# Kernel tuning notes

Hardware: AMD Instinct MI355X
Metric: run time of the kernel (lower is better)

## Reference

```python
import jax, jax.numpy as jnp
import numpy as np

B, S, D, H, E = 2, 1024, 1024, 4096, 8


def _xavier(key, shape):
    # matches torch.nn.init.xavier_uniform_ on a 3D tensor: fan_in/out from last two dims
    fan_in, fan_out = shape[-2], shape[-1]
    limit = float(np.sqrt(6.0 / (fan_in + fan_out)))
    return jax.random.uniform(key, shape, jnp.float32, -limit, limit)


def setup_inputs() -> dict:
    key = jax.random.key(0)
    ks = jax.random.split(key, 4)
    x = jax.random.normal(ks[0], (B, S, D), jnp.float32)
    router_w = jax.random.normal(ks[1], (D, E), jnp.float32) * (1.0 / np.sqrt(D))
    router_b = jnp.zeros((E,), jnp.float32)
    fc1_weight = _xavier(ks[2], (E, D, H))
    fc1_bias = jnp.zeros((E, H), jnp.float32)
    fc2_weight = _xavier(ks[3], (E, H, D))
    fc2_bias = jnp.zeros((E, D), jnp.float32)
    return {
        "x": x,
        "router_w": router_w,
        "router_b": router_b,
        "fc1_weight": fc1_weight,
        "fc1_bias": fc1_bias,
        "fc2_weight": fc2_weight,
        "fc2_bias": fc2_bias,
    }


def reference(x, router_w, router_b, fc1_weight, fc1_bias, fc2_weight, fc2_bias):
    b, s, d = x.shape
    x_flat = x.reshape(-1, d)                                  # [T, D]
    logits = x_flat @ router_w + router_b                       # [T, E]
    probs = jax.nn.softmax(logits, axis=-1)                     # [T, E]
    # per-expert FC1 + exact GELU (torch nn.GELU default is erf-based)
    h = jnp.einsum('td,edh->teh', x_flat, fc1_weight) + fc1_bias  # [T, E, H]
    h = jax.nn.gelu(h, approximate=False)
    expert_out = jnp.einsum('teh,ehd->ted', h, fc2_weight) + fc2_bias  # [T, E, D]
    out_flat = jnp.einsum('te,ted->td', probs, expert_out)      # [T, D]
    y = out_flat.reshape(b, s, d)
    router_probs = probs.reshape(b, s, -1)
    return y, router_probs
```

## Files before the change

kernel.cpp:

```cpp
#include <hip/hip_runtime.h>
#include <math.h>


typedef float f32x4 __attribute__((ext_vector_type(4)));
typedef __bf16 bf16x8 __attribute__((ext_vector_type(8)));

#define GLL16(gp, lp)                                                          \
  __builtin_amdgcn_global_load_lds(                                            \
      (const __attribute__((address_space(1))) void*)(gp),                     \
      (__attribute__((address_space(3))) void*)(lp), 16, 0, 0)

__device__ __forceinline__ float gelu_f(float h) {
  float x = h * 0.70710678118654752f;
  float ax = fabsf(x);
  float t = __builtin_amdgcn_rcpf(fmaf(0.3275911f, ax, 1.0f));
  float p = fmaf(1.061405429f, t, -1.453152027f);
  p = fmaf(p, t, 1.421413741f);
  p = fmaf(p, t, -0.284496736f);
  p = fmaf(p, t, 0.254829592f);
  float e = __expf(-x * x);
  float erfv = fmaf(-p * t, e, 1.0f);
  erfv = copysignf(erfv, x);
  return 0.5f * h * (1.0f + erfv);
}

__global__ void router_kernel(const float* __restrict__ x,
                              const float* __restrict__ rw,
                              const float* __restrict__ rb,
                              float* __restrict__ P,
                              float* __restrict__ probs_out)
{
  int gid = blockIdx.x * blockDim.x + threadIdx.x;
  int t = gid >> 6;
  int l = gid & 63;
  const float* xr = x + (size_t)t * 1024;
  float a[8];
#pragma unroll
  for (int e = 0; e < 8; ++e) a[e] = 0.f;
  for (int d = l; d < 1024; d += 64) {
    float xv = xr[d];
    f32x4 w0 = *(const f32x4*)(rw + d * 8);
    f32x4 w1 = *(const f32x4*)(rw + d * 8 + 4);
#pragma unroll
    for (int e = 0; e < 4; ++e) a[e] += xv * w0[e];
#pragma unroll
    for (int e = 0; e < 4; ++e) a[4 + e] += xv * w1[e];
  }
#pragma unroll
  for (int off = 32; off > 0; off >>= 1) {
#pragma unroll
    for (int e = 0; e < 8; ++e) a[e] += __shfl_down(a[e], off);
  }
  if (l == 0) {
#pragma unroll
    for (int e = 0; e < 8; ++e) a[e] += rb[e];
    float m = a[0];
#pragma unroll
    for (int e = 1; e < 8; ++e) m = fmaxf(m, a[e]);
    float s = 0.f;
#pragma unroll
    for (int e = 0; e < 8; ++e) { a[e] = __expf(a[e] - m); s += a[e]; }
    float inv = 1.f / s;
#pragma unroll
    for (int e = 0; e < 8; ++e) {
      float p = a[e] * inv;
      if (P) P[t * 8 + e] = p;
      probs_out[t * 8 + e] = p;
    }
  }
}

__global__ void cvt_kernel(const float* __restrict__ src,
                           __bf16* __restrict__ dst)
{
  size_t i = ((size_t)blockIdx.x * 256 + threadIdx.x) * 8;
  f32x4 v0 = *(const f32x4*)(src + i);
  f32x4 v1 = *(const f32x4*)(src + i + 4);
  bf16x8 o;
#pragma unroll
  for (int j = 0; j < 4; ++j) o[j] = (__bf16)v0[j];
#pragma unroll
  for (int j = 0; j < 4; ++j) o[4 + j] = (__bf16)v1[j];
  *(bf16x8*)(dst + i) = o;
}

__global__ void transconv_kernel(const float* __restrict__ src,
                                 __bf16* __restrict__ dst,
                                 int R, int C, size_t dstLd, size_t zOff)
{
  __shared__ float tile[64][65];
  size_t bs = (size_t)blockIdx.z * (size_t)R * (size_t)C;
  size_t dzo = (size_t)blockIdx.z * zOff;
  int r0 = blockIdx.x * 64, c0 = blockIdx.y * 64;
  int tr = threadIdx.x >> 4;
  int tc = (threadIdx.x & 15) * 4;
#pragma unroll
  for (int i = 0; i < 4; ++i) {
    f32x4 v = *(const f32x4*)(src + bs + (size_t)(r0 + tr + 16 * i) * C + c0 + tc);
#pragma unroll
    for (int j = 0; j < 4; ++j) tile[tr + 16 * i][tc + j] = v[j];
  }
  __syncthreads();
  int oc = threadIdx.x >> 3;
  int orr = (threadIdx.x & 7) * 8;
#pragma unroll
  for (int i = 0; i < 2; ++i) {
    int c = oc + 32 * i;
    bf16x8 o;
#pragma unroll
    for (int j = 0; j < 8; ++j) o[j] = (__bf16)tile[orr + j][c];
    *(bf16x8*)(dst + (size_t)(c0 + c) * dstLd + dzo + r0 + orr) = o;
  }
}

__device__ __forceinline__ void mfma_loop256(
    const char* Ab, const char* Bb, size_t ldaB, size_t ldbB, int K,
    char* lds, f32x4 acc[8][4])
{
  const int tid = threadIdx.x;
  const int w = tid >> 6, l = tid & 63;
  const int wm = w >> 2, wn = w & 3;
  const int m16 = l & 15, q = l >> 4;
  const int swz = m16 & 7;
  const int aBase = wm * 16384 + m16 * 128;
  const int bBase = 32768 + (wn >> 1) * 16384 + ((wn & 1) * 64 + m16) * 128;
  const int srcCh = ((l & 7) ^ ((l >> 3) & 7)) << 4;
  const size_t gA0 = (size_t)(w * 16 + (l >> 3)) * ldaB + srcCh;
  const size_t gB0 = (size_t)(w * 16 + (l >> 3)) * ldbB + srcCh;
  const int dstW = w * 2048;
  const int NT = K >> 6;

  bf16x8 af[4][2], bv[4][2];

#define STG_A(h, tau)                                                          \
  {                                                                            \
    char* d = lds + (((tau) & 1) * 65536) + (h) * 16384 + dstW;                \
    const char* g = Ab + gA0 + (size_t)((h) * 128) * ldaB + (size_t)(tau) * 128;\
    GLL16(g, d);                                                               \
    GLL16(g + 8 * ldaB, d + 1024);                                             \
  }
#define STG_B(h, tau)                                                          \
  {                                                                            \
    char* d = lds + (((tau) & 1) * 65536) + 32768 + (h) * 16384 + dstW;        \
    const char* g = Bb + gB0 + (size_t)((h) * 128) * ldbB + (size_t)(tau) * 128;\
    GLL16(g, d);                                                               \
    GLL16(g + 8 * ldbB, d + 1024);                                             \
  }
#define RD_A(lo, p)                                                            \
  _Pragma("unroll") for (int mi = 0; mi < 4; ++mi)                             \
  _Pragma("unroll") for (int ks = 0; ks < 2; ++ks)                             \
    af[mi][ks] = *(const bf16x8*)(lds + (p) * 65536 + aBase +                  \
        ((lo) * 4 + mi) * 2048 + (((ks * 4 + q) ^ swz) << 4));
#define RD_B(no, p)                                                            \
  _Pragma("unroll") for (int nj = 0; nj < 2; ++nj)                             \
  _Pragma("unroll") for (int ks = 0; ks < 2; ++ks)                             \
    bv[(no) * 2 + nj][ks] = *(const bf16x8*)(lds + (p) * 65536 + bBase +       \
        ((no) * 2 + nj) * 2048 + (((ks * 4 + q) ^ swz) << 4));
#define MM(lo, no)                                                             \
  __builtin_amdgcn_s_setprio(1);                                               \
  _Pragma("unroll") for (int mi = 0; mi < 4; ++mi)                             \
  _Pragma("unroll") for (int nj = 0; nj < 2; ++nj)                             \
  _Pragma("unroll") for (int ks = 0; ks < 2; ++ks)                             \
    acc[(lo) * 4 + mi][(no) * 2 + nj] =                                        \
        __builtin_amdgcn_mfma_f32_16x16x32_bf16(                               \
            af[mi][ks], bv[(no) * 2 + nj][ks],                                 \
            acc[(lo) * 4 + mi][(no) * 2 + nj], 0, 0, 0);                       \
  __builtin_amdgcn_s_setprio(0);
#define SB __builtin_amdgcn_sched_barrier(0)
#define BAR { SB; __builtin_amdgcn_s_barrier(); SB; }
#define VMW(n) asm volatile("s_waitcnt vmcnt(" #n ")" ::: "memory")

  STG_A(0, 0); STG_A(1, 0); STG_B(0, 0); STG_B(1, 0);
  STG_B(0, 1); STG_B(1, 1);
  VMW(4);
  BAR;

  int t = 0;
  for (; t < NT - 2; ++t) {
    const int p = t & 1;
    RD_A(0, p); RD_B(0, p);
    STG_A(0, t + 1);
    BAR; MM(0, 0); BAR;
    RD_B(1, p);
    STG_A(1, t + 1);
    BAR; MM(0, 1); BAR;
    RD_A(1, p);
    STG_B(0, t + 2);
    BAR; MM(1, 0); BAR;
    STG_B(1, t + 2);
    BAR; MM(1, 1); SB; VMW(4); BAR;
  }
  {
    const int p = t & 1;
    RD_A(0, p); RD_B(0, p);
    STG_A(0, t + 1);
    BAR; MM(0, 0); BAR;
    RD_B(1, p);
    STG_A(1, t + 1);
    BAR; MM(0, 1); BAR;
    RD_A(1, p);
    BAR; MM(1, 0); BAR;
    BAR; MM(1, 1); SB; VMW(0); BAR;
    ++t;
  }
  {
    const int p = t & 1;
    RD_A(0, p); RD_B(0, p);
    MM(0, 0);
    RD_B(1, p);
    MM(0, 1);
    RD_A(1, p);
    MM(1, 0);
    MM(1, 1);
  }
#undef STG_A
#undef STG_B
#undef RD_A
#undef RD_B
#undef MM
#undef SB
#undef BAR
#undef VMW
}

__device__ __forceinline__ int xcd_swz(int id, int nwg) {
  return ((nwg & 7) == 0) ? ((id & 7) * (nwg >> 3) + (id >> 3)) : id;
}

__global__ __launch_bounds__(512, 2) void gemm1_kernel(
    const __bf16* __restrict__ X, const __bf16* __restrict__ W1T,
    const float* __restrict__ b1, const float* __restrict__ P,
    __bf16* __restrict__ Hs, int hs_ld, int e_off, size_t b_zstride)
{
  __shared__ __align__(16) char lds[131072];
  const int nwg = gridDim.x * gridDim.y * gridDim.z;
  const int id = blockIdx.x + gridDim.x * (blockIdx.y + gridDim.y * blockIdx.z);
  const int wg = xcd_swz(id, nwg);
  const int bm = wg & 7;
  const int bn = (wg >> 3) % gridDim.y;
  const int z = wg / (gridDim.y << 3);
  const int e = z + e_off;

  f32x4 acc[8][4];
  const f32x4 z4 = {0.f, 0.f, 0.f, 0.f};
#pragma unroll
  for (int i = 0; i < 8; ++i)
#pragma unroll
    for (int j = 0; j < 4; ++j) acc[i][j] = z4;

  const char* A = (const char*)(X + (size_t)bm * 256 * 1024);
  const char* B = (const char*)(W1T + (size_t)z * b_zstride +
                                (size_t)bn * 256 * 1024);
  mfma_loop256(A, B, 2048, 2048, 1024, lds, acc);

  const int tid = threadIdx.x, w = tid >> 6, l = tid & 63;
  const int wm = w >> 2, wn = w & 3, q = l >> 4, m16 = l & 15;
  const int row0 = bm * 256 + wm * 128 + q * 4;
  const int colE = bn * 256 + wn * 64 + m16;
  const int zcol = (hs_ld == 4096) ? 0 : z * 4096;
  float b1v[4];
#pragma unroll
  for (int nj = 0; nj < 4; ++nj)
    b1v[nj] = b1[(size_t)e * 4096 + colE + nj * 16];
#pragma unroll
  for (int mi = 0; mi < 8; ++mi) {
    float pv[4];
#pragma unroll
    for (int r = 0; r < 4; ++r)
      pv[r] = P[(size_t)(row0 + mi * 16 + r) * 8 + e];
#pragma unroll
    for (int nj = 0; nj < 4; ++nj)
#pragma unroll
      for (int r = 0; r < 4; ++r) {
        float h = acc[mi][nj][r] + b1v[nj];
        float o = gelu_f(h) * pv[r];
        Hs[(size_t)(row0 + mi * 16 + r) * hs_ld + zcol + colE + nj * 16] =
            (__bf16)o;
      }
  }
}

__global__ __launch_bounds__(512, 2) void gemm2_kernel(
    const __bf16* __restrict__ Hs, const __bf16* __restrict__ W2T,
    float* __restrict__ accb, int lda, int ldb, int kz, int Kb)
{
  __shared__ __align__(16) char lds[131072];
  const int nwg = gridDim.x * gridDim.y * gridDim.z;
  const int id = blockIdx.x + gridDim.x * (blockIdx.y + gridDim.y * blockIdx.z);
  const int wg = xcd_swz(id, nwg);
  const int bm = wg & 7;
  const int bn = (wg >> 3) % gridDim.y;
  const int z = wg / (gridDim.y << 3);

  f32x4 acc[8][4];
  const f32x4 z4 = {0.f, 0.f, 0.f, 0.f};
#pragma unroll
  for (int i = 0; i < 8; ++i)
#pragma unroll
    for (int j = 0; j < 4; ++j) acc[i][j] = z4;

  const char* A = (const char*)(Hs + (size_t)bm * 256 * lda + (size_t)z * kz);
  const char* B = (const char*)(W2T + (size_t)bn * 256 * ldb + (size_t)z * kz);
  mfma_loop256(A, B, (size_t)lda * 2, (size_t)ldb * 2, Kb, lds, acc);

  const int tid = threadIdx.x, w = tid >> 6, l = tid & 63;
  const int wm = w >> 2, wn = w & 3, q = l >> 4, m16 = l & 15;
  const int row0 = bm * 256 + wm * 128 + q * 4;
  const int col0 = bn * 256 + wn * 64 + m16;
#pragma unroll
  for (int mi = 0; mi < 8; ++mi)
#pragma unroll
    for (int nj = 0; nj < 4; ++nj)
#pragma unroll
      for (int r = 0; r < 4; ++r)
        unsafeAtomicAdd(
            accb + (size_t)(row0 + mi * 16 + r) * 1024 + col0 + nj * 16,
            acc[mi][nj][r]);
}

__global__ void finalize_kernel(const float* __restrict__ accb,
                                const float* __restrict__ P,
                                const float* __restrict__ b2,
                                float* __restrict__ y)
{
  int idx = blockIdx.x * 256 + threadIdx.x;
  int t = idx >> 8;
  int d0 = (idx & 255) << 2;
  f32x4 a = *(const f32x4*)(accb + (size_t)t * 1024 + d0);
#pragma unroll
  for (int e = 0; e < 8; ++e) {
    float p = P[t * 8 + e];
    f32x4 b = *(const f32x4*)(b2 + (size_t)e * 1024 + d0);
#pragma unroll
    for (int c = 0; c < 4; ++c) a[c] += p * b[c];
  }
  *(f32x4*)(y + (size_t)t * 1024 + d0) = a;
}

__global__ __launch_bounds__(256) void fused_naive_kernel(
    const float* __restrict__ x, const float* __restrict__ w1,
    const float* __restrict__ b1, const float* __restrict__ w2,
    const float* __restrict__ b2, const float* __restrict__ probs,
    float* __restrict__ y)
{
  __shared__ float xs[8][1024];
  __shared__ float gs[8][64];
  __shared__ float ps[8];
  const int tid = threadIdx.x;
  const int t0 = blockIdx.x * 8;
  const size_t DH = (size_t)1024 * 4096;
  const int tt = tid >> 5;
  const int d0 = (tid & 31) * 32;
  float acc[32];
#pragma unroll
  for (int i = 0; i < 32; ++i) acc[i] = 0.f;
  {
    const f32x4* xsrc = (const f32x4*)(x + (size_t)t0 * 1024);
    f32x4* xdst = (f32x4*)&xs[0][0];
    for (int i = tid; i < 2048; i += 256) xdst[i] = xsrc[i];
  }
  const int wv = tid >> 6;
  const int hl = tid & 63;
  for (int e = 0; e < 8; ++e) {
    if (tid < 8) ps[tid] = probs[(size_t)(t0 + tid) * 8 + e];
    __syncthreads();
    for (int hc = 0; hc < 4096; hc += 64) {
      float a0 = 0.f, a1 = 0.f;
      const float* w1p = w1 + (size_t)e * DH + hc + hl;
      for (int d = 0; d < 1024; ++d) {
        float wvv = w1p[(size_t)d * 4096];
        a0 += xs[wv * 2 + 0][d] * wvv;
        a1 += xs[wv * 2 + 1][d] * wvv;
      }
      __syncthreads();
      gs[wv * 2 + 0][hl] =
          ps[wv * 2 + 0] * gelu_f(a0 + b1[(size_t)e * 4096 + hc + hl]);
      gs[wv * 2 + 1][hl] =
          ps[wv * 2 + 1] * gelu_f(a1 + b1[(size_t)e * 4096 + hc + hl]);
      __syncthreads();
      const float* w2p = w2 + (size_t)e * DH + (size_t)hc * 1024 + d0;
      for (int hh = 0; hh < 64; ++hh) {
        float g = gs[tt][hh];
#pragma unroll
        for (int jb = 0; jb < 8; ++jb) {
          f32x4 w4 = *(const f32x4*)(w2p + (size_t)hh * 1024 + jb * 4);
#pragma unroll
          for (int j2 = 0; j2 < 4; ++j2) acc[jb * 4 + j2] += g * w4[j2];
        }
      }
    }
#pragma unroll
    for (int j = 0; j < 32; ++j)
      acc[j] += ps[tt] * b2[(size_t)e * 1024 + d0 + j];
    __syncthreads();
  }
  float* yp = y + (size_t)(t0 + tt) * 1024 + d0;
#pragma unroll
  for (int jb = 0; jb < 8; ++jb) {
    f32x4 o = {acc[jb * 4], acc[jb * 4 + 1], acc[jb * 4 + 2], acc[jb * 4 + 3]};
    *(f32x4*)(yp + jb * 4) = o;
  }
}

extern "C" void kernel_launch(void* const* d_in, const int* in_sizes, int n_in,
                              void* d_out, int out_size, void* d_ws,
                              size_t ws_size, hipStream_t stream)
{
  const float* x  = (const float*)d_in[0];
  const float* rw = (const float*)d_in[1];
  const float* rb = (const float*)d_in[2];
  const float* w1 = (const float*)d_in[3];
  const float* b1 = (const float*)d_in[4];
  const float* w2 = (const float*)d_in[5];
  const float* b2 = (const float*)d_in[6];
  float* y = (float*)d_out;
  float* probs_out = y + (size_t)2048 * 1024;

  const size_t DH = (size_t)1024 * 4096;
  const size_t BASE = (64 << 10) + (size_t)2048 * 1024 * 4 +
                      (size_t)2048 * 1024 * 2;
  const size_t TA = BASE + 8 * DH * 2 + (size_t)2048 * 32768 * 2;
  const size_t TB = BASE + DH * 2 + (size_t)2048 * 4096 * 2;

  char* ws = (char*)d_ws;
  float* P = (float*)ws;
  float* accb = (float*)(ws + (64 << 10));
  __bf16* xb = (__bf16*)(ws + (64 << 10) + (size_t)2048 * 1024 * 4);
  char* ws2 = ws + BASE;

  if (ws_size >= TA) {
    router_kernel<<<512, 256, 0, stream>>>(x, rw, rb, P, probs_out);
    hipMemsetAsync(accb, 0, (size_t)2048 * 1024 * 4, stream);
    cvt_kernel<<<1024, 256, 0, stream>>>(x, xb);
    __bf16* WT = (__bf16*)ws2;
    __bf16* Hs = WT + 8 * DH;
    transconv_kernel<<<dim3(16, 64, 8), 256, 0, stream>>>(
        w1, WT, 1024, 4096, 1024, DH);
    gemm1_kernel<<<dim3(8, 16, 8), 512, 0, stream>>>(xb, WT, b1, P, Hs,
                                                     32768, 0, DH);
    transconv_kernel<<<dim3(64, 16, 8), 256, 0, stream>>>(
        w2, WT, 4096, 1024, 32768, 4096);
    gemm2_kernel<<<dim3(8, 4, 8), 512, 0, stream>>>(Hs, WT, accb, 32768,
                                                    32768, 4096, 4096);
    finalize_kernel<<<2048, 256, 0, stream>>>(accb, P, b2, y);
  } else if (ws_size >= TB) {
    router_kernel<<<512, 256, 0, stream>>>(x, rw, rb, P, probs_out);
    hipMemsetAsync(accb, 0, (size_t)2048 * 1024 * 4, stream);
    cvt_kernel<<<1024, 256, 0, stream>>>(x, xb);
    __bf16* WT = (__bf16*)ws2;
    __bf16* HsE = WT + DH;
    for (int e = 0; e < 8; ++e) {
      transconv_kernel<<<dim3(16, 64, 1), 256, 0, stream>>>(
          w1 + e * DH, WT, 1024, 4096, 1024, 0);
      gemm1_kernel<<<dim3(8, 16, 1), 512, 0, stream>>>(xb, WT, b1, P, HsE,
                                                       4096, e, 0);
      transconv_kernel<<<dim3(64, 16, 1), 256, 0, stream>>>(
          w2 + e * DH, WT, 4096, 1024, 4096, 0);
      gemm2_kernel<<<dim3(8, 4, 4), 512, 0, stream>>>(HsE, WT, accb, 4096,
                                                      4096, 1024, 1024);
    }
    finalize_kernel<<<2048, 256, 0, stream>>>(accb, P, b2, y);
  } else {
    router_kernel<<<512, 256, 0, stream>>>(x, rw, rb, (float*)nullptr,
                                           probs_out);
    fused_naive_kernel<<<256, 256, 0, stream>>>(x, w1, b1, w2, b2, probs_out,
                                                y);
  }
}
```

Baseline: 620.0 us.

## Fuse fp32 weight transpose-convert into GEMM B-operand loading

Removes the separate transconv kernels that transposed and converted fc1/fc2 weights to bf16 in workspace. The GEMM mainloop now loads fp32 weights straight from global memory into registers, converts them to bf16 and writes them transposed into swizzled LDS, with a new pipelining schedule and waitcnt placement. This avoids writing and rereading the transposed weight copies and saves workspace. In exchange, B loads become per-thread scalar fp32 loads instead of direct-to-LDS loads, which adds register pressure and VALU work inside the MFMA loop.

```diff
diff --git a/kernel.cpp b/kernel.cpp
--- a/kernel.cpp
+++ b/kernel.cpp
@@ -84,52 +84,25 @@
   *(bf16x8*)(dst + i) = o;
 }
 
-__global__ void transconv_kernel(const float* __restrict__ src,
-                                 __bf16* __restrict__ dst,
-                                 int R, int C, size_t dstLd, size_t zOff)
-{
-  __shared__ float tile[64][65];
-  size_t bs = (size_t)blockIdx.z * (size_t)R * (size_t)C;
-  size_t dzo = (size_t)blockIdx.z * zOff;
-  int r0 = blockIdx.x * 64, c0 = blockIdx.y * 64;
-  int tr = threadIdx.x >> 4;
-  int tc = (threadIdx.x & 15) * 4;
-#pragma unroll
-  for (int i = 0; i < 4; ++i) {
-    f32x4 v = *(const f32x4*)(src + bs + (size_t)(r0 + tr + 16 * i) * C + c0 + tc);
-#pragma unroll
-    for (int j = 0; j < 4; ++j) tile[tr + 16 * i][tc + j] = v[j];
-  }
-  __syncthreads();
-  int oc = threadIdx.x >> 3;
-  int orr = (threadIdx.x & 7) * 8;
-#pragma unroll
-  for (int i = 0; i < 2; ++i) {
-    int c = oc + 32 * i;
-    bf16x8 o;
-#pragma unroll
-    for (int j = 0; j < 8; ++j) o[j] = (__bf16)tile[orr + j][c];
-    *(bf16x8*)(dst + (size_t)(c0 + c) * dstLd + dzo + r0 + orr) = o;
-  }
-}
-
 __device__ __forceinline__ void mfma_loop256(
-    const char* Ab, const char* Bb, size_t ldaB, size_t ldbB, int K,
+    const char* Ab, const float* Bf, size_t ldaB, int ldN, int K,
     char* lds, f32x4 acc[8][4])
 {
   const int tid = threadIdx.x;
   const int w = tid >> 6, l = tid & 63;
   const int wm = w >> 2, wn = w & 3;
   const int m16 = l & 15, q = l >> 4;
-  const int swz = m16 & 7;
+  const int s1 = m16 & 7, s2 = m16 >> 3;
   const int aBase = wm * 16384 + m16 * 128;
-  const int bBase = 32768 + (wn >> 1) * 16384 + ((wn & 1) * 64 + m16) * 128;
+  const int bRow = 32768 + (wn >> 1) * 16384 + ((wn & 1) * 64 + m16) * 128;
   const int srcCh = ((l & 7) ^ ((l >> 3) & 7)) << 4;
   const size_t gA0 = (size_t)(w * 16 + (l >> 3)) * ldaB + srcCh;
-  const size_t gB0 = (size_t)(w * 16 + (l >> 3)) * ldbB + srcCh;
   const int dstW = w * 2048;
+  const float* bThr = Bf + (size_t)(w * 8) * (size_t)ldN + l;
+  const int bwBase = 32768 + l * 128 + ((w ^ ((l & 7) ^ ((l >> 3) & 7))) << 4);
   const int NT = K >> 6;
 
+  float bq0[8], bq1[8];
   bf16x8 af[4][2], bv[4][2];
 
 #define STG_A(h, tau)                                                          \
@@ -139,23 +112,27 @@
     GLL16(g, d);                                                               \
     GLL16(g + 8 * ldaB, d + 1024);                                             \
   }
-#define STG_B(h, tau)                                                          \
+#define BL_Q(arr, j, tau)                                                      \
+  _Pragma("unroll") for (int kk = 0; kk < 8; ++kk)                             \
+    arr[kk] = bThr[((size_t)(tau) * 64 + kk) * (size_t)ldN + (j) * 64];
+#define BW_Q(arr, j, tau)                                                      \
   {                                                                            \
-    char* d = lds + (((tau) & 1) * 65536) + 32768 + (h) * 16384 + dstW;        \
-    const char* g = Bb + gB0 + (size_t)((h) * 128) * ldbB + (size_t)(tau) * 128;\
-    GLL16(g, d);                                                               \
-    GLL16(g + 8 * ldbB, d + 1024);                                             \
+    bf16x8 vv;                                                                 \
+    _Pragma("unroll") for (int kk = 0; kk < 8; ++kk) vv[kk] = (__bf16)arr[kk]; \
+    *(bf16x8*)(lds + (((tau) & 1) * 65536) + bwBase + (j) * 8192) = vv;        \
   }
 #define RD_A(lo, p)                                                            \
   _Pragma("unroll") for (int mi = 0; mi < 4; ++mi)                             \
   _Pragma("unroll") for (int ks = 0; ks < 2; ++ks)                             \
     af[mi][ks] = *(const bf16x8*)(lds + (p) * 65536 + aBase +                  \
-        ((lo) * 4 + mi) * 2048 + (((ks * 4 + q) ^ swz) << 4));
+        ((lo) * 4 + mi) * 2048 + (((ks * 4 + q) ^ s1) << 4));
 #define RD_B(no, p)                                                            \
-  _Pragma("unroll") for (int nj = 0; nj < 2; ++nj)                             \
-  _Pragma("unroll") for (int ks = 0; ks < 2; ++ks)                             \
-    bv[(no) * 2 + nj][ks] = *(const bf16x8*)(lds + (p) * 65536 + bBase +       \
-        ((no) * 2 + nj) * 2048 + (((ks * 4 + q) ^ swz) << 4));
+  _Pragma("unroll") for (int nj = 0; nj < 2; ++nj) {                           \
+    const int fB = s1 ^ ((((no) * 2 + nj) * 2 + s2) & 7);                      \
+    _Pragma("unroll") for (int ks = 0; ks < 2; ++ks)                           \
+      bv[(no) * 2 + nj][ks] = *(const bf16x8*)(lds + (p) * 65536 + bRow +      \
+          ((no) * 2 + nj) * 2048 + (((ks * 4 + q) ^ fB) << 4));                \
+  }
 #define MM(lo, no)                                                             \
   __builtin_amdgcn_s_setprio(1);                                               \
   _Pragma("unroll") for (int mi = 0; mi < 4; ++mi)                             \
@@ -169,38 +146,66 @@
 #define SB __builtin_amdgcn_sched_barrier(0)
 #define BAR { SB; __builtin_amdgcn_s_barrier(); SB; }
 #define VMW(n) asm volatile("s_waitcnt vmcnt(" #n ")" ::: "memory")
-
-  STG_A(0, 0); STG_A(1, 0); STG_B(0, 0); STG_B(1, 0);
-  STG_B(0, 1); STG_B(1, 1);
-  VMW(4);
+#define LKW0 asm volatile("s_waitcnt lgkmcnt(0)" ::: "memory")
+
+  STG_A(0, 0); STG_A(1, 0);
+  BL_Q(bq0, 0, 0); BL_Q(bq1, 1, 0);
+  VMW(0);
+  BW_Q(bq0, 0, 0); BW_Q(bq1, 1, 0);
+  BL_Q(bq0, 2, 0); BL_Q(bq1, 3, 0);
+  VMW(0);
+  BW_Q(bq0, 2, 0); BW_Q(bq1, 3, 0);
+  BL_Q(bq0, 0, 1); BL_Q(bq1, 1, 1);
+  VMW(0);
+  BW_Q(bq0, 0, 1); BW_Q(bq1, 1, 1);
+  BL_Q(bq0, 2, 1); BL_Q(bq1, 3, 1);
+  LKW0;
   BAR;
 
   int t = 0;
   for (; t < NT - 2; ++t) {
     const int p = t & 1;
     RD_A(0, p); RD_B(0, p);
+    VMW(8);
+    BW_Q(bq0, 2, t + 1);
+    BL_Q(bq0, 0, t + 2);
     STG_A(0, t + 1);
     BAR; MM(0, 0); BAR;
     RD_B(1, p);
+    VMW(10);
+    BW_Q(bq1, 3, t + 1);
+    BL_Q(bq1, 1, t + 2);
     STG_A(1, t + 1);
     BAR; MM(0, 1); BAR;
     RD_A(1, p);
-    STG_B(0, t + 2);
+    VMW(10);
+    BW_Q(bq0, 0, t + 2);
+    BL_Q(bq0, 2, t + 2);
     BAR; MM(1, 0); BAR;
-    STG_B(1, t + 2);
-    BAR; MM(1, 1); SB; VMW(4); BAR;
+    VMW(8);
+    BW_Q(bq1, 1, t + 2);
+    BL_Q(bq1, 3, t + 2);
+    BAR; MM(1, 1); SB;
+    LKW0;
+    BAR;
   }
   {
     const int p = t & 1;
     RD_A(0, p); RD_B(0, p);
+    VMW(8);
+    BW_Q(bq0, 2, t + 1);
     STG_A(0, t + 1);
     BAR; MM(0, 0); BAR;
     RD_B(1, p);
+    VMW(2);
+    BW_Q(bq1, 3, t + 1);
     STG_A(1, t + 1);
     BAR; MM(0, 1); BAR;
     RD_A(1, p);
     BAR; MM(1, 0); BAR;
-    BAR; MM(1, 1); SB; VMW(0); BAR;
+    MM(1, 1); SB;
+    asm volatile("s_waitcnt vmcnt(0) lgkmcnt(0)" ::: "memory");
+    BAR;
     ++t;
   }
   {
@@ -214,13 +219,15 @@
     MM(1, 1);
   }
 #undef STG_A
-#undef STG_B
+#undef BL_Q
+#undef BW_Q
 #undef RD_A
 #undef RD_B
 #undef MM
 #undef SB
 #undef BAR
 #undef VMW
+#undef LKW0
 }
 
 __device__ __forceinline__ int xcd_swz(int id, int nwg) {
@@ -228,7 +235,7 @@
 }
 
 __global__ __launch_bounds__(512, 2) void gemm1_kernel(
-    const __bf16* __restrict__ X, const __bf16* __restrict__ W1T,
+    const __bf16* __restrict__ X, const float* __restrict__ W1,
     const float* __restrict__ b1, const float* __restrict__ P,
     __bf16* __restrict__ Hs, int hs_ld, int e_off, size_t b_zstride)
 {
@@ -249,9 +256,8 @@
     for (int j = 0; j < 4; ++j) acc[i][j] = z4;
 
   const char* A = (const char*)(X + (size_t)bm * 256 * 1024);
-  const char* B = (const char*)(W1T + (size_t)z * b_zstride +
-                                (size_t)bn * 256 * 1024);
-  mfma_loop256(A, B, 2048, 2048, 1024, lds, acc);
+  const float* Bf = W1 + (size_t)z * b_zstride + (size_t)bn * 256;
+  mfma_loop256(A, Bf, 2048, 4096, 1024, lds, acc);
 
   const int tid = threadIdx.x, w = tid >> 6, l = tid & 63;
   const int wm = w >> 2, wn = w & 3, q = l >> 4, m16 = l & 15;
@@ -281,8 +287,8 @@
 }
 
 __global__ __launch_bounds__(512, 2) void gemm2_kernel(
-    const __bf16* __restrict__ Hs, const __bf16* __restrict__ W2T,
-    float* __restrict__ accb, int lda, int ldb, int kz, int Kb)
+    const __bf16* __restrict__ Hs, const float* __restrict__ W2,
+    float* __restrict__ accb, int lda, size_t a_zoff, size_t b_zoff, int Kb)
 {
   __shared__ __align__(16) char lds[131072];
   const int nwg = gridDim.x * gridDim.y * gridDim.z;
@@ -299,9 +305,9 @@
 #pragma unroll
     for (int j = 0; j < 4; ++j) acc[i][j] = z4;
 
-  const char* A = (const char*)(Hs + (size_t)bm * 256 * lda + (size_t)z * kz);
-  const char* B = (const char*)(W2T + (size_t)bn * 256 * ldb + (size_t)z * kz);
-  mfma_loop256(A, B, (size_t)lda * 2, (size_t)ldb * 2, Kb, lds, acc);
+  const char* A = (const char*)(Hs + (size_t)bm * 256 * lda + (size_t)z * a_zoff);
+  const float* Bf = W2 + (size_t)z * b_zoff + (size_t)bn * 256;
+  mfma_loop256(A, Bf, (size_t)lda * 2, 1024, Kb, lds, acc);
 
   const int tid = threadIdx.x, w = tid >> 6, l = tid & 63;
   const int wm = w >> 2, wn = w & 3, q = l >> 4, m16 = l & 15;
@@ -419,45 +425,34 @@
   const size_t DH = (size_t)1024 * 4096;
   const size_t BASE = (64 << 10) + (size_t)2048 * 1024 * 4 +
                       (size_t)2048 * 1024 * 2;
-  const size_t TA = BASE + 8 * DH * 2 + (size_t)2048 * 32768 * 2;
-  const size_t TB = BASE + DH * 2 + (size_t)2048 * 4096 * 2;
+  const size_t TA = BASE + (size_t)2048 * 32768 * 2;
+  const size_t TB = BASE + (size_t)2048 * 4096 * 2;
 
   char* ws = (char*)d_ws;
   float* P = (float*)ws;
   float* accb = (float*)(ws + (64 << 10));
   __bf16* xb = (__bf16*)(ws + (64 << 10) + (size_t)2048 * 1024 * 4);
-  char* ws2 = ws + BASE;
+  __bf16* Hs = (__bf16*)(ws + BASE);
 
   if (ws_size >= TA) {
     router_kernel<<<512, 256, 0, stream>>>(x, rw, rb, P, probs_out);
     hipMemsetAsync(accb, 0, (size_t)2048 * 1024 * 4, stream);
     cvt_kernel<<<1024, 256, 0, stream>>>(x, xb);
-    __bf16* WT = (__bf16*)ws2;
-    __bf16* Hs = WT + 8 * DH;
-    transconv_kernel<<<dim3(16, 64, 8), 256, 0, stream>>>(
-        w1, WT, 1024, 4096, 1024, DH);
-    gemm1_kernel<<<dim3(8, 16, 8), 512, 0, stream>>>(xb, WT, b1, P, Hs,
+    gemm1_kernel<<<dim3(8, 16, 8), 512, 0, stream>>>(xb, w1, b1, P, Hs,
                                                      32768, 0, DH);
-    transconv_kernel<<<dim3(64, 16, 8), 256, 0, stream>>>(
-        w2, WT, 4096, 1024, 32768, 4096);
-    gemm2_kernel<<<dim3(8, 4, 8), 512, 0, stream>>>(Hs, WT, accb, 32768,
-                                                    32768, 4096, 4096);
+    gemm2_kernel<<<dim3(8, 4, 8), 512, 0, stream>>>(Hs, w2, accb, 32768,
+                                                    4096, DH, 4096);
     finalize_kernel<<<2048, 256, 0, stream>>>(accb, P, b2, y);
   } else if (ws_size >= TB) {
     router_kernel<<<512, 256, 0, stream>>>(x, rw, rb, P, probs_out);
     hipMemsetAsync(accb, 0, (size_t)2048 * 1024 * 4, stream);
     cvt_kernel<<<1024, 256, 0, stream>>>(x, xb);
-    __bf16* WT = (__bf16*)ws2;
-    __bf16* HsE = WT + DH;
     for (int e = 0; e < 8; ++e) {
-      transconv_kernel<<<dim3(16, 64, 1), 256, 0, stream>>>(
-          w1 + e * DH, WT, 1024, 4096, 1024, 0);
-      gemm1_kernel<<<dim3(8, 16, 1), 512, 0, stream>>>(xb, WT, b1, P, HsE,
-                                                       4096, e, 0);
-      transconv_kernel<<<dim3(64, 16, 1), 256, 0, stream>>>(
-          w2 + e * DH, WT, 4096, 1024, 4096, 0);
-      gemm2_kernel<<<dim3(8, 4, 4), 512, 0, stream>>>(HsE, WT, accb, 4096,
-                                                      4096, 1024, 1024);
+      gemm1_kernel<<<dim3(8, 16, 1), 512, 0, stream>>>(
+          xb, w1 + (size_t)e * DH, b1, P, Hs, 4096, e, 0);
+      gemm2_kernel<<<dim3(8, 4, 4), 512, 0, stream>>>(
+          Hs, w2 + (size_t)e * DH, accb, 4096, 1024,
+          (size_t)1024 * 1024, 1024);
     }
     finalize_kernel<<<2048, 256, 0, stream>>>(accb, P, b2, y);
   } else {
```

After: 922.7 us. +48.8%, slower.
